# Kernel optimization log

Measured on AMD Instinct MI355X. Metric: run time of the kernel, lower is better.

The kernel has to match this reference:

```python
import jax, jax.numpy as jnp
import numpy as np

B, T, C, H = 4, 2048, 1024, 16
D = C // H  # head_dim = 64


def setup_inputs() -> dict:
    key = jax.random.key(0)
    k1, k2, k3, k4 = jax.random.split(key, 4)
    x = jax.random.normal(k1, (B, T, C), dtype=jnp.float32)
    # realistic padding: each sequence has length in [T//2, T]
    lengths = jax.random.randint(k4, (B,), T // 2, T + 1)
    padding_mask = jnp.arange(T)[None, :] < lengths[:, None]  # True = keep
    # weights stored [in, out] (equivalent to torch Linear weight transposed)
    w_qkv = jax.random.normal(k2, (C, 3 * C), dtype=jnp.float32) * (C ** -0.5)
    w_out = jax.random.normal(k3, (C, C), dtype=jnp.float32) * (C ** -0.5)
    b_out = jnp.zeros((C,), dtype=jnp.float32)
    return {"x": x, "padding_mask": padding_mask, "w_qkv": w_qkv, "w_out": w_out, "b_out": b_out}


def reference(x, padding_mask, w_qkv, w_out, b_out):
    scale = D ** -0.5
    qkv = x @ w_qkv  # [B,T,3C]
    q, k, v = jnp.split(qkv, 3, axis=-1)

    def split_heads(t):
        return t.reshape(B, T, H, D).transpose(0, 2, 1, 3)  # [B,H,T,D]

    q, k, v = split_heads(q), split_heads(k), split_heads(v)
    attn = jnp.einsum("bhqd,bhkd->bhqk", q, k) * scale  # [B,H,T,T]
    mask = padding_mask[:, None, None, :]  # [B,1,1,T]
    attn = jnp.where(mask, attn, jnp.finfo(attn.dtype).min)
    attn = jax.nn.softmax(attn, axis=-1)
    # dropout is identity in eval mode
    out = jnp.einsum("bhqk,bhkd->bhqd", attn, v)  # [B,H,T,D]
    out = out.transpose(0, 2, 1, 3).reshape(B, T, C)
    return out @ w_out + b_out
```

## Files before the change

### kernel.cpp

```cpp
#include <hip/hip_runtime.h>
#include <hip/hip_bf16.h>

#define Bb 4
#define Tt 2048
#define Cc 1024
#define Hh 16

typedef unsigned short u16;
typedef __attribute__((ext_vector_type(8))) __bf16 bf16x8;
typedef __attribute__((ext_vector_type(4))) float  f32x4;

__device__ __forceinline__ u16 f2bf_hw(float f) {
    __bf16 h = (__bf16)f;
    return *(u16*)&h;
}

__device__ __forceinline__ unsigned cvt_pk_bf16(float a, float b) {
    unsigned r;
    asm("v_cvt_pk_bf16_f32 %0, %1, %2" : "=v"(r) : "v"(a), "v"(b));
    return r;
}

__device__ __forceinline__ float fexp2(float x) {
#if __has_builtin(__builtin_amdgcn_exp2f)
    return __builtin_amdgcn_exp2f(x);
#else
    return __expf(x * 0.6931471805599453f);
#endif
}

__device__ __forceinline__ void gld_lds16(const void* g, void* l) {
    __builtin_amdgcn_global_load_lds(
        (__attribute__((address_space(1))) void*)(g),
        (__attribute__((address_space(3))) void*)(l),
        16, 0, 0);
}

__device__ __forceinline__ f32x4 mfma16(bf16x8 a, bf16x8 b, f32x4 c) {
    return __builtin_amdgcn_mfma_f32_16x16x32_bf16(a, b, c, 0, 0, 0);
}

__global__ void cast_f32_bf16(const float* __restrict__ in, u16* __restrict__ out, int n4) {
    int i = blockIdx.x * 256 + threadIdx.x;
    if (i < n4) {
        float4 v = ((const float4*)in)[i];
        uint2 o;
        o.x = cvt_pk_bf16(v.x, v.y);
        o.y = cvt_pk_bf16(v.z, v.w);
        ((uint2*)out)[i] = o;
    }
}

__global__ void castT_f32_bf16(const float* __restrict__ in, u16* __restrict__ out,
                               int K, int N, int scaleN, float sv) {
    __shared__ float Ls[64][65];
    const int n0 = blockIdx.x * 64, k0 = blockIdx.y * 64;
    const int t = threadIdx.x;
    #pragma unroll
    for (int s = 0; s < 4; ++s) {
        int idx = t + 256 * s;
        int r   = idx >> 4;
        int c4  = (idx & 15) * 4;
        float4 v = *(const float4*)&in[(size_t)(k0 + r) * N + n0 + c4];
        Ls[r][c4 + 0] = v.x; Ls[r][c4 + 1] = v.y;
        Ls[r][c4 + 2] = v.z; Ls[r][c4 + 3] = v.w;
    }
    __syncthreads();
    #pragma unroll
    for (int s = 0; s < 2; ++s) {
        int idx = t + 256 * s;
        int n   = idx >> 3;
        int kc  = (idx & 7) * 8;
        const float sc = (n0 + n < scaleN) ? sv : 1.0f;
        alignas(16) u16 tmp[8];
        #pragma unroll
        for (int i = 0; i < 8; ++i) tmp[i] = f2bf_hw(Ls[kc + i][n] * sc);
        *(uint4*)&out[(size_t)(n0 + n) * K + k0 + kc] = *(const uint4*)tmp;
    }
}

__global__ __launch_bounds__(256, 3) void gemm_bt_bf16(
    const u16* __restrict__ A, const u16* __restrict__ Bt,
    const float* __restrict__ bias,
    u16* __restrict__ outB, float* __restrict__ outF,
    int M, int N, int K)
{
    __shared__ u16 As[128 * 32];
    __shared__ u16 Bs[128 * 32];
    const int t = threadIdx.x;
    const int w = t >> 6, lane = t & 63;
    const int quad = lane >> 4, l16 = lane & 15;
    const int wr = w >> 1, wc = w & 1;
    const int m0 = blockIdx.y * 128, n0 = blockIdx.x * 128;

    int aoff[4], boff[4];
    #pragma unroll
    for (int i = 0; i < 4; ++i) {
        int rA = 64 * wr + 16 * i + l16;
        aoff[i] = rA * 32 + ((quad ^ ((rA >> 1) & 3)) * 8);
        int rB = 64 * wc + 16 * i + l16;
        boff[i] = rB * 32 + ((quad ^ ((rB >> 1) & 3)) * 8);
    }

    f32x4 acc[4][4] = {};

    for (int k0 = 0; k0 < K; k0 += 32) {
        __syncthreads();
        #pragma unroll
        for (int u = 0; u < 2; ++u) {
            const int i   = 2 * w + u;
            const int row = 16 * i + (lane >> 2);
            const int c   = (lane & 3) ^ ((row >> 1) & 3);
            gld_lds16(A  + (size_t)(m0 + row) * K + k0 + c * 8, (void*)(As + i * 512 + lane * 8));
            gld_lds16(Bt + (size_t)(n0 + row) * K + k0 + c * 8, (void*)(Bs + i * 512 + lane * 8));
        }
        asm volatile("s_waitcnt vmcnt(0)" ::: "memory");
        __syncthreads();

        bf16x8 af[4], bfr[4];
        #pragma unroll
        for (int i = 0; i < 4; ++i) af[i]  = *(const bf16x8*)&As[aoff[i]];
        #pragma unroll
        for (int j = 0; j < 4; ++j) bfr[j] = *(const bf16x8*)&Bs[boff[j]];
        #pragma unroll
        for (int i = 0; i < 4; ++i)
            #pragma unroll
            for (int j = 0; j < 4; ++j)
                acc[i][j] = mfma16(af[i], bfr[j], acc[i][j]);
    }

    const int rbase = m0 + 64 * wr + quad * 4;
    const int cbase = n0 + 64 * wc + l16;
    if (outF) {
        float bv[4];
        #pragma unroll
        for (int j = 0; j < 4; ++j) bv[j] = bias[cbase + 16 * j];
        #pragma unroll
        for (int i = 0; i < 4; ++i)
            #pragma unroll
            for (int r = 0; r < 4; ++r) {
                size_t ro = (size_t)(rbase + 16 * i + r) * N;
                #pragma unroll
                for (int j = 0; j < 4; ++j)
                    outF[ro + cbase + 16 * j] = acc[i][j][r] + bv[j];
            }
    } else {
        #pragma unroll
        for (int i = 0; i < 4; ++i)
            #pragma unroll
            for (int r = 0; r < 4; ++r) {
                size_t ro = (size_t)(rbase + 16 * i + r) * N;
                #pragma unroll
                for (int j = 0; j < 4; ++j)
                    outB[ro + cbase + 16 * j] = f2bf_hw(acc[i][j][r]);
            }
    }
}

__global__ __launch_bounds__(256, 3) void gemm_qkv_bt(
    const u16* __restrict__ A, const u16* __restrict__ Bt,
    u16* __restrict__ outQ, u16* __restrict__ kx, u16* __restrict__ vx)
{
    const int M = Bb * Tt, N = 3 * Cc, K = Cc;
    __shared__ u16 As[128 * 32];
    __shared__ u16 Bs[128 * 32];
    const int t = threadIdx.x;
    const int w = t >> 6, lane = t & 63;
    const int quad = lane >> 4, l16 = lane & 15;
    const int wr = w >> 1, wc = w & 1;
    const int m0 = blockIdx.y * 128, n0 = blockIdx.x * 128;
    (void)M; (void)N;

    int aoff[4], boff[4];
    #pragma unroll
    for (int i = 0; i < 4; ++i) {
        int rA = 64 * wr + 16 * i + l16;
        aoff[i] = rA * 32 + ((quad ^ ((rA >> 1) & 3)) * 8);
        int rB = 64 * wc + 16 * i + l16;
        boff[i] = rB * 32 + ((quad ^ ((rB >> 1) & 3)) * 8);
    }

    f32x4 acc[4][4] = {};

    for (int k0 = 0; k0 < K; k0 += 32) {
        __syncthreads();
        #pragma unroll
        for (int u = 0; u < 2; ++u) {
            const int i   = 2 * w + u;
            const int row = 16 * i + (lane >> 2);
            const int c   = (lane & 3) ^ ((row >> 1) & 3);
            gld_lds16(A  + (size_t)(m0 + row) * K + k0 + c * 8, (void*)(As + i * 512 + lane * 8));
            gld_lds16(Bt + (size_t)(n0 + row) * K + k0 + c * 8, (void*)(Bs + i * 512 + lane * 8));
        }
        asm volatile("s_waitcnt vmcnt(0)" ::: "memory");
        __syncthreads();

        bf16x8 af[4], bfr[4];
        #pragma unroll
        for (int i = 0; i < 4; ++i) af[i]  = *(const bf16x8*)&As[aoff[i]];
        #pragma unroll
        for (int j = 0; j < 4; ++j) bfr[j] = *(const bf16x8*)&Bs[boff[j]];
        #pragma unroll
        for (int i = 0; i < 4; ++i)
            #pragma unroll
            for (int j = 0; j < 4; ++j)
                acc[i][j] = mfma16(af[i], bfr[j], acc[i][j]);
    }

    const int rbase = m0 + 64 * wr + quad * 4;
    const int cbase = n0 + 64 * wc + l16;
    const int region = n0 >> 10;

    if (region == 0) {
        #pragma unroll
        for (int i = 0; i < 4; ++i)
            #pragma unroll
            for (int r = 0; r < 4; ++r) {
                size_t ro = (size_t)(rbase + 16 * i + r) * Cc;
                #pragma unroll
                for (int j = 0; j < 4; ++j)
                    outQ[ro + cbase + 16 * j] = f2bf_hw(acc[i][j][r]);
            }
    } else if (region == 1) {
        int colK[4];
        #pragma unroll
        for (int j = 0; j < 4; ++j) {
            const int c = (cbase - 1024) + 16 * j;
            const int h = c >> 6, d = c & 63;
            colK[j] = h * 131072 + (d >> 5) * 512 + ((d >> 3) & 3) * 128 + (d & 7);
        }
        #pragma unroll
        for (int i = 0; i < 4; ++i)
            #pragma unroll
            for (int r = 0; r < 4; ++r) {
                const int row = rbase + 16 * i + r;
                const int b = row >> 11, key = row & 2047;
                const int ch = key >> 6, keyr = key & 63;
                const int rowK = b * 2097152 + ch * 4096 + (keyr >> 4) * 1024 + (keyr & 15) * 8;
                #pragma unroll
                for (int j = 0; j < 4; ++j)
                    kx[rowK + colK[j]] = f2bf_hw(acc[i][j][r]);
            }
    } else {
        int colV[4];
        #pragma unroll
        for (int j = 0; j < 4; ++j) {
            const int c = (cbase - 2048) + 16 * j;
            const int h = c >> 6, d = c & 63;
            colV[j] = h * 131072 + (d >> 4) * 1024 + (d & 15) * 8;
        }
        #pragma unroll
        for (int i = 0; i < 4; ++i)
            #pragma unroll
            for (int r = 0; r < 4; ++r) {
                const int row = rbase + 16 * i + r;
                const int b = row >> 11, key = row & 2047;
                const int ch = key >> 6, keyr = key & 63;
                const int rowV = b * 2097152 + ch * 4096 + (keyr >> 5) * 512
                               + ((keyr >> 3) & 3) * 128 + (keyr & 7);
                #pragma unroll
                for (int j = 0; j < 4; ++j)
                    vx[rowV + colV[j]] = f2bf_hw(acc[i][j][r]);
            }
    }
}

__global__ __launch_bounds__(256, 2) void attn_mfma4(
    const u16* __restrict__ qb, const u16* __restrict__ kx, const u16* __restrict__ vx,
    const int* __restrict__ mask, u16* __restrict__ outO)
{
    __shared__ u16 KVs[8192];
    __shared__ u16 Pss[4][16 * 68];

    const int t = threadIdx.x;
    const int w = t >> 6, lane = t & 63;
    const int quad = lane >> 4, l16 = lane & 15;
    const int bh = blockIdx.x, qblk = blockIdx.y, b = bh >> 4, h = bh & 15;

    int sum = 0;
    {
        const int4* mp = (const int4*)(mask + b * Tt) + lane * 8;
        #pragma unroll
        for (int i = 0; i < 8; ++i) { int4 m4 = mp[i]; sum += m4.x + m4.y + m4.z + m4.w; }
        #pragma unroll
        for (int off = 1; off < 64; off <<= 1) sum += __shfl_xor(sum, off);
    }
    const int L = sum;

    const int q0 = qblk * 256 + w * 64;
    bf16x8 qf[4][2];
    #pragma unroll
    for (int qq = 0; qq < 4; ++qq) {
        const u16* qp = qb + (size_t)(b * Tt + q0 + 16 * qq + l16) * Cc + h * 64 + quad * 8;
        qf[qq][0] = *(const bf16x8*)(qp);
        qf[qq][1] = *(const bf16x8*)(qp + 32);
    }

    f32x4 oacc[4][4] = {};
    f32x4 lacc[4]    = {};
    const __bf16 onebf = (__bf16)1.0f;
    const bf16x8 ones  = {onebf, onebf, onebf, onebf, onebf, onebf, onebf, onebf};

    const int nfull = L >> 6;
    const int nch   = (L + 63) >> 6;
    const size_t cb0 = (size_t)bh * 32 * 4096;
    u16* Pw = Pss[w];

    {
        uint4 k0a = *(const uint4*)&kx[cb0 + t * 8];
        uint4 k0b = *(const uint4*)&kx[cb0 + 2048 + t * 8];
        uint4 v0a = *(const uint4*)&vx[cb0 + t * 8];
        uint4 v0b = *(const uint4*)&vx[cb0 + 2048 + t * 8];
        *(uint4*)&KVs[t * 8]        = k0a;
        *(uint4*)&KVs[2048 + t * 8] = k0b;
        *(uint4*)&KVs[4096 + t * 8] = v0a;
        *(uint4*)&KVs[6144 + t * 8] = v0b;
    }
    __syncthreads();

    for (int ch = 0; ch < nch; ++ch) {
        const int cc = (ch + 1 < nch) ? ch + 1 : ch;
        const size_t nb = cb0 + (size_t)cc * 4096;
        uint4 nk0 = *(const uint4*)&kx[nb + t * 8];
        uint4 nk1 = *(const uint4*)&kx[nb + 2048 + t * 8];
        uint4 nv0 = *(const uint4*)&vx[nb + t * 8];
        uint4 nv1 = *(const uint4*)&vx[nb + 2048 + t * 8];

        const u16* Kb = KVs;
        const u16* Vb = KVs + 4096;

        bf16x8 kf[4][2];
        #pragma unroll
        for (int jt = 0; jt < 4; ++jt)
            #pragma unroll
            for (int ks = 0; ks < 2; ++ks)
                kf[jt][ks] = *(const bf16x8*)&Kb[(jt * 2 + ks) * 512 + lane * 8];

        bf16x8 vf[4][2];
        #pragma unroll
        for (int dt = 0; dt < 4; ++dt)
            #pragma unroll
            for (int ks = 0; ks < 2; ++ks)
                vf[dt][ks] = *(const bf16x8*)&Vb[(dt * 2 + ks) * 512 + lane * 8];

        #pragma unroll
        for (int qq = 0; qq < 4; ++qq) {
            f32x4 st[4];
            #pragma unroll
            for (int jt = 0; jt < 4; ++jt) {
                f32x4 z = {0.f, 0.f, 0.f, 0.f};
                z = mfma16(kf[jt][0], qf[qq][0], z);
                st[jt] = mfma16(kf[jt][1], qf[qq][1], z);
            }
            uint2 pk[4];
            if (ch < nfull) {
                #pragma unroll
                for (int jt = 0; jt < 4; ++jt) {
                    pk[jt].x = cvt_pk_bf16(fexp2(st[jt][0]), fexp2(st[jt][1]));
                    pk[jt].y = cvt_pk_bf16(fexp2(st[jt][2]), fexp2(st[jt][3]));
                }
            } else {
                const int kc = ch * 64;
                #pragma unroll
                for (int jt = 0; jt < 4; ++jt) {
                    const int kb = kc + 16 * jt + quad * 4;
                    float e[4];
                    #pragma unroll
                    for (int r = 0; r < 4; ++r)
                        e[r] = (kb + r < L) ? fexp2(st[jt][r]) : 0.f;
                    pk[jt].x = cvt_pk_bf16(e[0], e[1]);
                    pk[jt].y = cvt_pk_bf16(e[2], e[3]);
                }
            }
            #pragma unroll
            for (int jt = 0; jt < 4; ++jt)
                *(uint2*)&Pw[l16 * 68 + 16 * jt + quad * 4] = pk[jt];

            #pragma unroll
            for (int ks = 0; ks < 2; ++ks) {
                const u16* pr = &Pw[l16 * 68 + 32 * ks + quad * 8];
                uint2 pa = *(const uint2*)pr;
                uint2 pb = *(const uint2*)(pr + 4);
                uint4 comb = {pa.x, pa.y, pb.x, pb.y};
                bf16x8 pf = *(const bf16x8*)&comb;
                #pragma unroll
                for (int dt = 0; dt < 4; ++dt)
                    oacc[qq][dt] = mfma16(pf, vf[dt][ks], oacc[qq][dt]);
                lacc[qq] = mfma16(pf, ones, lacc[qq]);
            }
        }

        __syncthreads();
        *(uint4*)&KVs[t * 8]        = nk0;
        *(uint4*)&KVs[2048 + t * 8] = nk1;
        *(uint4*)&KVs[4096 + t * 8] = nv0;
        *(uint4*)&KVs[6144 + t * 8] = nv1;
        __syncthreads();
    }

    #pragma unroll
    for (int qq = 0; qq < 4; ++qq)
        #pragma unroll
        for (int r = 0; r < 4; ++r) {
            const float inv = 1.f / lacc[qq][r];
            const size_t ro = (size_t)(b * Tt + q0 + 16 * qq + quad * 4 + r) * Cc + h * 64 + l16;
            #pragma unroll
            for (int dt = 0; dt < 4; ++dt)
                outO[ro + 16 * dt] = f2bf_hw(oacc[qq][dt][r] * inv);
        }
}

extern "C" void kernel_launch(void* const* d_in, const int* in_sizes, int n_in,
                              void* d_out, int out_size, void* d_ws, size_t ws_size,
                              hipStream_t stream) {
    const float* x     = (const float*)d_in[0];
    const int*   mask  = (const int*)  d_in[1];
    const float* w_qkv = (const float*)d_in[2];
    const float* w_out = (const float*)d_in[3];
    const float* b_out = (const float*)d_in[4];
    float*       outp  = (float*)d_out;

    const int M = Bb * Tt;
    char* ws = (char*)d_ws;
    u16* xb     = (u16*)(ws);
    u16* wqkvT  = (u16*)(ws + (16u << 20));
    u16* woutT  = (u16*)(ws + (22u << 20));
    u16* qbuf   = (u16*)(ws + (24u << 20));
    u16* kx     = (u16*)(ws + (40u << 20));
    u16* vx     = (u16*)(ws + (56u << 20));
    u16* attnO  = (u16*)(ws);

    const float c2 = 0.18033688011112042f;

    cast_f32_bf16<<<(M * Cc / 4 + 255) / 256, 256, 0, stream>>>(x, xb, M * Cc / 4);
    castT_f32_bf16<<<dim3(3 * Cc / 64, Cc / 64), 256, 0, stream>>>(w_qkv, wqkvT, Cc, 3 * Cc, Cc, c2);
    castT_f32_bf16<<<dim3(Cc / 64, Cc / 64), 256, 0, stream>>>(w_out, woutT, Cc, Cc, 0, 1.0f);

    gemm_qkv_bt<<<dim3(3 * Cc / 128, M / 128), 256, 0, stream>>>(
        xb, wqkvT, qbuf, kx, vx);

    attn_mfma4<<<dim3(Bb * Hh, Tt / 256), 256, 0, stream>>>(qbuf, kx, vx, mask, attnO);

    gemm_bt_bf16<<<dim3(Cc / 128, M / 128), 256, 0, stream>>>(
        attnO, woutT, b_out, nullptr, outp, M, Cc, Cc);
}
```

Measured before the change: 260.9 us.

## Double GEMM K-tile to 64 with 8-way XOR swizzle and setprio around attention MFMAs

Both bf16 GEMM kernels now stage a 64-wide K slice per iteration instead of 32, halving the number of barrier/wait rounds per output tile. The loader addressing is rebuilt with precomputed per-thread row pointers and an 8-way XOR swizzle to suit the wider row, and each tile is processed as two 32-wide substeps. The attention kernel also raises wave priority around its MFMA blocks so they can be issued ahead of other waves. LDS use doubles, which may reduce occupancy below the launch-bounds target.

New measurement: 241.9 us. -7.3%, faster.

```diff
diff --git a/kernel.cpp b/kernel.cpp
--- a/kernel.cpp
+++ b/kernel.cpp
@@ -85,52 +85,66 @@
     u16* __restrict__ outB, float* __restrict__ outF,
     int M, int N, int K)
 {
-    __shared__ u16 As[128 * 32];
-    __shared__ u16 Bs[128 * 32];
+    __shared__ u16 As[128 * 64];
+    __shared__ u16 Bs[128 * 64];
     const int t = threadIdx.x;
     const int w = t >> 6, lane = t & 63;
     const int quad = lane >> 4, l16 = lane & 15;
-    const int wr = w >> 1, wc = w & 1;
+    const int wm = w >> 1, wn = w & 1;
     const int m0 = blockIdx.y * 128, n0 = blockIdx.x * 128;
 
-    int aoff[4], boff[4];
+    const int l8r   = lane >> 3;
+    const int g_log = (lane & 7) ^ l8r;
+    const u16* sAp[4]; const u16* sBp[4];
+    #pragma unroll
+    for (int u = 0; u < 4; ++u) {
+        const int gi = w * 4 + u;
+        sAp[u] = A  + (size_t)(m0 + gi * 8 + l8r) * K + g_log * 8;
+        sBp[u] = Bt + (size_t)(n0 + gi * 8 + l8r) * K + g_log * 8;
+    }
+    const int dst0 = w * 2048 + lane * 8;
+
+    int aoff[4][2], boff[4][2];
     #pragma unroll
     for (int i = 0; i < 4; ++i) {
-        int rA = 64 * wr + 16 * i + l16;
-        aoff[i] = rA * 32 + ((quad ^ ((rA >> 1) & 3)) * 8);
-        int rB = 64 * wc + 16 * i + l16;
-        boff[i] = rB * 32 + ((quad ^ ((rB >> 1) & 3)) * 8);
+        const int rA = 64 * wm + 16 * i + l16;
+        const int rB = 64 * wn + 16 * i + l16;
+        #pragma unroll
+        for (int kk = 0; kk < 2; ++kk) {
+            aoff[i][kk] = rA * 64 + (((4 * kk + quad) ^ (rA & 7)) * 8);
+            boff[i][kk] = rB * 64 + (((4 * kk + quad) ^ (rB & 7)) * 8);
+        }
     }
 
     f32x4 acc[4][4] = {};
 
-    for (int k0 = 0; k0 < K; k0 += 32) {
-        __syncthreads();
-        #pragma unroll
-        for (int u = 0; u < 2; ++u) {
-            const int i   = 2 * w + u;
-            const int row = 16 * i + (lane >> 2);
-            const int c   = (lane & 3) ^ ((row >> 1) & 3);
-            gld_lds16(A  + (size_t)(m0 + row) * K + k0 + c * 8, (void*)(As + i * 512 + lane * 8));
-            gld_lds16(Bt + (size_t)(n0 + row) * K + k0 + c * 8, (void*)(Bs + i * 512 + lane * 8));
+    for (int k0 = 0; k0 < K; k0 += 64) {
+        __syncthreads();
+        #pragma unroll
+        for (int u = 0; u < 4; ++u) {
+            gld_lds16(sAp[u] + k0, (void*)(As + dst0 + u * 512));
+            gld_lds16(sBp[u] + k0, (void*)(Bs + dst0 + u * 512));
         }
         asm volatile("s_waitcnt vmcnt(0)" ::: "memory");
         __syncthreads();
 
-        bf16x8 af[4], bfr[4];
-        #pragma unroll
-        for (int i = 0; i < 4; ++i) af[i]  = *(const bf16x8*)&As[aoff[i]];
-        #pragma unroll
-        for (int j = 0; j < 4; ++j) bfr[j] = *(const bf16x8*)&Bs[boff[j]];
-        #pragma unroll
-        for (int i = 0; i < 4; ++i)
-            #pragma unroll
-            for (int j = 0; j < 4; ++j)
-                acc[i][j] = mfma16(af[i], bfr[j], acc[i][j]);
-    }
-
-    const int rbase = m0 + 64 * wr + quad * 4;
-    const int cbase = n0 + 64 * wc + l16;
+        #pragma unroll
+        for (int kk = 0; kk < 2; ++kk) {
+            bf16x8 af[4], bfr[4];
+            #pragma unroll
+            for (int i = 0; i < 4; ++i) af[i]  = *(const bf16x8*)&As[aoff[i][kk]];
+            #pragma unroll
+            for (int j = 0; j < 4; ++j) bfr[j] = *(const bf16x8*)&Bs[boff[j][kk]];
+            #pragma unroll
+            for (int i = 0; i < 4; ++i)
+                #pragma unroll
+                for (int j = 0; j < 4; ++j)
+                    acc[i][j] = mfma16(af[i], bfr[j], acc[i][j]);
+        }
+    }
+
+    const int rbase = m0 + 64 * wm + quad * 4;
+    const int cbase = n0 + 64 * wn + l16;
     if (outF) {
         float bv[4];
         #pragma unroll
@@ -161,54 +175,67 @@
     const u16* __restrict__ A, const u16* __restrict__ Bt,
     u16* __restrict__ outQ, u16* __restrict__ kx, u16* __restrict__ vx)
 {
-    const int M = Bb * Tt, N = 3 * Cc, K = Cc;
-    __shared__ u16 As[128 * 32];
-    __shared__ u16 Bs[128 * 32];
+    const int K = Cc;
+    __shared__ u16 As[128 * 64];
+    __shared__ u16 Bs[128 * 64];
     const int t = threadIdx.x;
     const int w = t >> 6, lane = t & 63;
     const int quad = lane >> 4, l16 = lane & 15;
-    const int wr = w >> 1, wc = w & 1;
+    const int wm = w >> 1, wn = w & 1;
     const int m0 = blockIdx.y * 128, n0 = blockIdx.x * 128;
-    (void)M; (void)N;
-
-    int aoff[4], boff[4];
+
+    const int l8r   = lane >> 3;
+    const int g_log = (lane & 7) ^ l8r;
+    const u16* sAp[4]; const u16* sBp[4];
+    #pragma unroll
+    for (int u = 0; u < 4; ++u) {
+        const int gi = w * 4 + u;
+        sAp[u] = A  + (size_t)(m0 + gi * 8 + l8r) * K + g_log * 8;
+        sBp[u] = Bt + (size_t)(n0 + gi * 8 + l8r) * K + g_log * 8;
+    }
+    const int dst0 = w * 2048 + lane * 8;
+
+    int aoff[4][2], boff[4][2];
     #pragma unroll
     for (int i = 0; i < 4; ++i) {
-        int rA = 64 * wr + 16 * i + l16;
-        aoff[i] = rA * 32 + ((quad ^ ((rA >> 1) & 3)) * 8);
-        int rB = 64 * wc + 16 * i + l16;
-        boff[i] = rB * 32 + ((quad ^ ((rB >> 1) & 3)) * 8);
+        const int rA = 64 * wm + 16 * i + l16;
+        const int rB = 64 * wn + 16 * i + l16;
+        #pragma unroll
+        for (int kk = 0; kk < 2; ++kk) {
+            aoff[i][kk] = rA * 64 + (((4 * kk + quad) ^ (rA & 7)) * 8);
+            boff[i][kk] = rB * 64 + (((4 * kk + quad) ^ (rB & 7)) * 8);
+        }
     }
 
     f32x4 acc[4][4] = {};
 
-    for (int k0 = 0; k0 < K; k0 += 32) {
-        __syncthreads();
-        #pragma unroll
-        for (int u = 0; u < 2; ++u) {
-            const int i   = 2 * w + u;
-            const int row = 16 * i + (lane >> 2);
-            const int c   = (lane & 3) ^ ((row >> 1) & 3);
-            gld_lds16(A  + (size_t)(m0 + row) * K + k0 + c * 8, (void*)(As + i * 512 + lane * 8));
-            gld_lds16(Bt + (size_t)(n0 + row) * K + k0 + c * 8, (void*)(Bs + i * 512 + lane * 8));
+    for (int k0 = 0; k0 < K; k0 += 64) {
+        __syncthreads();
+        #pragma unroll
+        for (int u = 0; u < 4; ++u) {
+            gld_lds16(sAp[u] + k0, (void*)(As + dst0 + u * 512));
+            gld_lds16(sBp[u] + k0, (void*)(Bs + dst0 + u * 512));
         }
         asm volatile("s_waitcnt vmcnt(0)" ::: "memory");
         __syncthreads();
 
-        bf16x8 af[4], bfr[4];
-        #pragma unroll
-        for (int i = 0; i < 4; ++i) af[i]  = *(const bf16x8*)&As[aoff[i]];
-        #pragma unroll
-        for (int j = 0; j < 4; ++j) bfr[j] = *(const bf16x8*)&Bs[boff[j]];
-        #pragma unroll
-        for (int i = 0; i < 4; ++i)
-            #pragma unroll
-            for (int j = 0; j < 4; ++j)
-                acc[i][j] = mfma16(af[i], bfr[j], acc[i][j]);
-    }
-
-    const int rbase = m0 + 64 * wr + quad * 4;
-    const int cbase = n0 + 64 * wc + l16;
+        #pragma unroll
+        for (int kk = 0; kk < 2; ++kk) {
+            bf16x8 af[4], bfr[4];
+            #pragma unroll
+            for (int i = 0; i < 4; ++i) af[i]  = *(const bf16x8*)&As[aoff[i][kk]];
+            #pragma unroll
+            for (int j = 0; j < 4; ++j) bfr[j] = *(const bf16x8*)&Bs[boff[j][kk]];
+            #pragma unroll
+            for (int i = 0; i < 4; ++i)
+                #pragma unroll
+                for (int j = 0; j < 4; ++j)
+                    acc[i][j] = mfma16(af[i], bfr[j], acc[i][j]);
+        }
+    }
+
+    const int rbase = m0 + 64 * wm + quad * 4;
+    const int cbase = n0 + 64 * wn + l16;
     const int region = n0 >> 10;
 
     if (region == 0) {
@@ -346,12 +373,14 @@
         #pragma unroll
         for (int qq = 0; qq < 4; ++qq) {
             f32x4 st[4];
+            __builtin_amdgcn_s_setprio(1);
             #pragma unroll
             for (int jt = 0; jt < 4; ++jt) {
                 f32x4 z = {0.f, 0.f, 0.f, 0.f};
                 z = mfma16(kf[jt][0], qf[qq][0], z);
                 st[jt] = mfma16(kf[jt][1], qf[qq][1], z);
             }
+            __builtin_amdgcn_s_setprio(0);
             uint2 pk[4];
             if (ch < nfull) {
                 #pragma unroll
@@ -376,6 +405,7 @@
             for (int jt = 0; jt < 4; ++jt)
                 *(uint2*)&Pw[l16 * 68 + 16 * jt + quad * 4] = pk[jt];
 
+            __builtin_amdgcn_s_setprio(1);
             #pragma unroll
             for (int ks = 0; ks < 2; ++ks) {
                 const u16* pr = &Pw[l16 * 68 + 32 * ks + quad * 8];
@@ -388,6 +418,7 @@
                     oacc[qq][dt] = mfma16(pf, vf[dt][ks], oacc[qq][dt]);
                 lacc[qq] = mfma16(pf, ones, lacc[qq]);
             }
+            __builtin_amdgcn_s_setprio(0);
         }
 
         __syncthreads();
```
